# Optimization experiments

Measured on AMD Instinct MI355X. Metric: run time of the kernel, lower is better.

The kernel has to match this reference:

```python
import jax, jax.numpy as jnp
import numpy as np

P = 128; D = 128; A = 128
NS = D * A            # sinogram nodes
NP = P * P            # pixel nodes
N = NS + NP           # total graph nodes
EPS = 1e-5
_PNAMES = ["af_w1","af_b1","af_p1","af_bn_g","af_bn_b","af_w2","af_b2","af_p2","af_w3","af_b3","af_p3","af_w4","af_b4","af_p4","af_w5","af_b5","af_p5","gcn_w","gcn_b","sr_w1","sr_b1","sr_p1","sr_w2","sr_b2","sr_p2","sr_w3","sr_b3","sr_p3"]


def _conv(x, w, b, pad):
    y = jax.lax.conv_general_dilated(x, w, (1, 1), [(pad, pad), (pad, pad)],
                                     dimension_numbers=("NCHW", "OIHW", "NCHW"))
    return y + b[None, :, None, None]


def _prelu(x, a):
    return jnp.where(x >= 0, x, a * x)


def _bn(x, g, b):
    # BatchNorm2d in training mode: biased batch stats over (N,H,W)
    m = x.mean(axis=(0, 2, 3), keepdims=True)
    v = x.var(axis=(0, 2, 3), keepdims=True)
    return (x - m) * jax.lax.rsqrt(v + EPS) * g[None, :, None, None] + b[None, :, None, None]


def _forward(sino, edge_index, edge_weight, p):
    # AndrewCNN sinogram filter: 1 -> 64 -> 64 -> 64 -> 64 -> 8, 7x7 convs
    h = _prelu(_conv(sino, p["af_w1"], p["af_b1"], 3), p["af_p1"])
    h = _bn(h, p["af_bn_g"], p["af_bn_b"])
    h = _prelu(_conv(h, p["af_w2"], p["af_b2"], 3), p["af_p2"])
    h = _prelu(_conv(h, p["af_w3"], p["af_b3"], 3), p["af_p3"])
    h = _prelu(_conv(h, p["af_w4"], p["af_b4"], 3), p["af_p4"])
    h = _prelu(_conv(h, p["af_w5"], p["af_b5"], 3), p["af_p5"])   # [B,8,D,A]
    B, F = h.shape[0], h.shape[1]
    # build_nodes_features (source_to_target): sino nodes first, zero pixel nodes
    flat_sino = h.transpose(0, 2, 3, 1).reshape(B, NS, F)
    x = jnp.concatenate([flat_sino, jnp.zeros((B, NP, F), h.dtype)], axis=1)  # [B,N,8]
    # GCNConv(8,10): lin -> gcn_norm with self loops -> scatter-add at targets -> +bias
    xl = x @ p["gcn_w"]                                            # [B,N,10]
    row, col = edge_index[0], edge_index[1]
    loop = jnp.arange(N)
    row2 = jnp.concatenate([row, loop])
    col2 = jnp.concatenate([col, loop])
    w2 = jnp.concatenate([edge_weight, jnp.ones((N,), edge_weight.dtype)])
    deg = jnp.zeros((N,), xl.dtype).at[col2].add(w2)
    dis = jnp.where(deg > 0, jax.lax.rsqrt(jnp.maximum(deg, EPS * 0 + 1e-30)), 0.0)
    norm = dis[row2] * w2 * dis[col2]                              # [E+N]
    msgs = xl[:, row2, :] * norm[None, :, None]                    # [B,E+N,10]
    agg = jnp.zeros_like(xl).at[:, col2, :].add(msgs) + p["gcn_b"]
    # keep pixel nodes, reshape to image grid
    img = agg[:, NS:, :].transpose(0, 2, 1).reshape(B, -1, P, P)   # [B,10,P,P]
    # SRNET: 10 -> 64 (9x9) -> 32 (1x1) -> 1 (5x5)
    o = _prelu(_conv(img, p["sr_w1"], p["sr_b1"], 4), p["sr_p1"])
    o = _prelu(_conv(o,   p["sr_w2"], p["sr_b2"], 0), p["sr_p2"])
    o = _prelu(_conv(o,   p["sr_w3"], p["sr_b3"], 2), p["sr_p3"])
    return o


def setup_inputs() -> dict:
    f = jnp.float32
    ks = jax.random.split(jax.random.key(0), 16)
    B, E = 4, 2097152
    def rn(k, shape, s):
        return jax.random.normal(k, shape, f) * s
    inp = {
        "sino": jax.random.normal(ks[0], (B, 1, D, A), f),
        "edge_index": jax.random.randint(ks[1], (2, E), 0, N),
        "edge_weight": jax.random.uniform(ks[2], (E,), f),
    }
    kw = jax.random.split(ks[3], 9)
    inp["af_w1"] = rn(kw[0], (64, 1, 7, 7), 0.2)
    inp["af_w2"] = rn(kw[1], (64, 64, 7, 7), 0.03)
    inp["af_w3"] = rn(kw[2], (64, 64, 7, 7), 0.03)
    inp["af_w4"] = rn(kw[3], (64, 64, 7, 7), 0.03)
    inp["af_w5"] = rn(kw[4], (8, 64, 7, 7), 0.03)
    inp["gcn_w"] = rn(kw[5], (8, 10), 0.3)
    inp["sr_w1"] = rn(kw[6], (64, 10, 9, 9), 0.05)
    inp["sr_w2"] = rn(kw[7], (32, 64, 1, 1), 0.18)
    inp["sr_w3"] = rn(kw[8], (1, 32, 5, 5), 0.05)
    for nm, c in [("af_b1", 64), ("af_b2", 64), ("af_b3", 64), ("af_b4", 64), ("af_b5", 8), ("sr_b1", 64), ("sr_b2", 32), ("sr_b3", 1)]:
        inp[nm] = jnp.zeros((c,), f)
    inp["gcn_b"] = jnp.zeros((10,), f)
    inp["af_bn_g"] = jnp.ones((64,), f)
    inp["af_bn_b"] = jnp.zeros((64,), f)
    for nm in ["af_p1", "af_p2", "af_p3", "af_p4", "af_p5", "sr_p1", "sr_p2", "sr_p3"]:
        inp[nm] = jnp.array(0.25, f)
    return inp


def reference(sino, edge_index, edge_weight, af_w1, af_b1, af_p1, af_bn_g, af_bn_b, af_w2, af_b2, af_p2, af_w3, af_b3, af_p3, af_w4, af_b4, af_p4, af_w5, af_b5, af_p5, gcn_w, gcn_b, sr_w1, sr_b1, sr_p1, sr_w2, sr_b2, sr_p2, sr_w3, sr_b3, sr_p3):
    p = dict(zip(_PNAMES, (af_w1, af_b1, af_p1, af_bn_g, af_bn_b, af_w2, af_b2, af_p2, af_w3, af_b3, af_p3, af_w4, af_b4, af_p4, af_w5, af_b5, af_p5, gcn_w, gcn_b, sr_w1, sr_b1, sr_p1, sr_w2, sr_b2, sr_p2, sr_w3, sr_b3, sr_p3)))
    return _forward(sino, edge_index, edge_weight, p)
```

## Files before the change

kernel.cpp:

```cpp
#include <hip/hip_runtime.h>

static constexpr int NS = 16384;

typedef __attribute__((ext_vector_type(8))) short bf16x8;
typedef __attribute__((ext_vector_type(4))) float f32x4;

__device__ inline unsigned short bf16_rne(float x) {
  unsigned u = __float_as_uint(x);
  unsigned r = u + 0x7FFF + ((u >> 16) & 1);
  return (unsigned short)(r >> 16);
}

__global__ void k_wtrans(const float* __restrict__ w, float* __restrict__ wT,
                         int CO, int CI_IN, int CI_OUT, int KS) {
  int i = blockIdx.x * 256 + threadIdx.x;
  int tot = KS * KS * CI_OUT * CO;
  if (i >= tot) return;
  int co = i % CO;
  int r = i / CO;
  int ci = r % CI_OUT;
  int t = r / CI_OUT;
  int ky = t / KS, kx = t % KS;
  float v = 0.f;
  if (ci < CI_IN) v = w[((co * CI_IN + ci) * KS + ky) * KS + kx];
  wT[i] = v;
}

__global__ void k_wpack(const float* __restrict__ w, unsigned short* __restrict__ wpk) {
  int i = blockIdx.x * 256 + threadIdx.x;
  if (i >= 49 * 64 * 64) return;
  int co = i & 63, r = i >> 6;
  int ci = r & 63, tap = r >> 6;
  float v = w[(co * 64 + ci) * 49 + tap];
  unsigned short hi = bf16_rne(v);
  float hif = __uint_as_float((unsigned)hi << 16);
  unsigned short lo = bf16_rne(v - hif);
  int ks = ci >> 5, k32 = ci & 31;
  int lane = ((k32 >> 3) << 4) | (co & 15);
  int j = ci & 7, nt = co >> 4;
  size_t base = ((size_t)(((tap * 2 + ks) * 4 + nt) * 2) * 64 + lane) * 8 + j;
  wpk[base] = hi;
  wpk[base + 512] = lo;
}

__global__ void k_wpacks(const float* __restrict__ sw1,
                         unsigned short* __restrict__ wpk) {
  int i = blockIdx.x * 256 + threadIdx.x;
  if (i >= 360 * 512) return;
  int j = i & 7, l = (i >> 3) & 63, f = i >> 9;
  int sp = f & 1, nt = (f >> 1) & 3;
  int r3 = f >> 3, p = r3 % 5, ky = r3 / 5;
  int co = nt * 16 + (l & 15);
  int k = ((l >> 4) << 3) + j;
  int kx = 2 * p + (k >> 4);
  int ci = k & 15;
  float v = (ci < 10 && kx < 9) ? sw1[((co * 10 + ci) * 9 + ky) * 9 + kx] : 0.f;
  unsigned short hi = bf16_rne(v);
  unsigned short outv;
  if (sp == 0) {
    outv = hi;
  } else {
    float hif = __uint_as_float((unsigned)hi << 16);
    outv = bf16_rne(v - hif);
  }
  wpk[i] = outv;
}

__global__ __launch_bounds__(128) void k_conv1(
    const float* __restrict__ sino, const float* __restrict__ wT1,
    const float* __restrict__ b1, const float* __restrict__ p1,
    float* __restrict__ out) {
  int b = blockIdx.x >> 7, y = blockIdx.x & 127, x = threadIdx.x;
  float acc[64];
#pragma unroll
  for (int i = 0; i < 64; ++i) acc[i] = 0.f;
#pragma unroll
  for (int ky = 0; ky < 7; ++ky) {
    int yy = y + ky - 3;
#pragma unroll
    for (int kx = 0; kx < 7; ++kx) {
      int xx = x + kx - 3;
      float v = (yy >= 0 && yy < 128 && xx >= 0 && xx < 128)
                    ? sino[(b * 128 + yy) * 128 + xx]
                    : 0.f;
      const float* wr = wT1 + (ky * 7 + kx) * 64;
#pragma unroll
      for (int co = 0; co < 64; ++co) acc[co] += v * wr[co];
    }
  }
  float a = p1[0];
  float* op = out + ((size_t)(b * 134 + y + 3) * 134 + x + 3) * 64;
#pragma unroll
  for (int co = 0; co < 64; ++co) {
    float v = acc[co] + b1[co];
    op[co] = v >= 0.f ? v : a * v;
  }
}

__global__ __launch_bounds__(256) void k_bnstats(const float* __restrict__ x1p,
                                                 double* __restrict__ bnsum) {
  int c = threadIdx.x & 63, sl = threadIdx.x >> 6;
  double s = 0.0, q = 0.0;
  int base = blockIdx.x * 512 + sl * 128;
  for (int i = 0; i < 128; ++i) {
    int p = base + i;
    int b = p >> 14, y = (p >> 7) & 127, x = p & 127;
    double v = (double)x1p[((size_t)(b * 134 + y + 3) * 134 + x + 3) * 64 + c];
    s += v;
    q += v * v;
  }
  __shared__ double red[2][4][64];
  red[0][sl][c] = s;
  red[1][sl][c] = q;
  __syncthreads();
  if (sl == 0) {
    s = red[0][0][c] + red[0][1][c] + red[0][2][c] + red[0][3][c];
    q = red[1][0][c] + red[1][1][c] + red[1][2][c] + red[1][3][c];
    atomicAdd(&bnsum[c], s);
    atomicAdd(&bnsum[64 + c], q);
  }
}

__global__ void k_bnfinal(const double* __restrict__ bnsum, float* __restrict__ bnsc,
                          const float* __restrict__ g, const float* __restrict__ bb) {
  int c = threadIdx.x;
  if (c >= 64) return;
  double m = bnsum[c] * (1.0 / 65536.0);
  double v = bnsum[64 + c] * (1.0 / 65536.0) - m * m;
  double sc = (double)g[c] * rsqrt(v + 1e-5);
  bnsc[c] = (float)sc;
  bnsc[64 + c] = (float)((double)bb[c] - m * sc);
}

__global__ __launch_bounds__(256) void k_bnapply(float* __restrict__ x1p,
                                                 const float* __restrict__ bnsc) {
  int i = blockIdx.x * 256 + threadIdx.x;
  if (i >= 4 * 128 * 128 * 16) return;
  int g = i & 15, p = i >> 4;
  int b = p >> 14, y = (p >> 7) & 127, x = p & 127;
  float* ptr = x1p + ((size_t)(b * 134 + y + 3) * 134 + x + 3) * 64 + g * 4;
  float4 v = *(float4*)ptr;
  int c = g * 4;
  v.x = v.x * bnsc[c + 0] + bnsc[64 + c + 0];
  v.y = v.y * bnsc[c + 1] + bnsc[64 + c + 1];
  v.z = v.z * bnsc[c + 2] + bnsc[64 + c + 2];
  v.w = v.w * bnsc[c + 3] + bnsc[64 + c + 3];
  *(float4*)ptr = v;
}

__global__ __launch_bounds__(256) void k_convm(
    const float* __restrict__ in, const unsigned short* __restrict__ wpk,
    const float* __restrict__ bias, const float* __restrict__ alpha,
    float* __restrict__ out) {
  int b = blockIdx.x >> 7, y = blockIdx.x & 127;
  int tid = threadIdx.x, l = tid & 63;
  int wv = tid >> 6;
  int wbase = wv * 32;
  int lg = l >> 4, lm = l & 15;

  __shared__ unsigned short hbuf[2][134 * 40];
  __shared__ unsigned short lbuf[2][134 * 40];

  f32x4 acc[2][4];
#pragma unroll
  for (int mt = 0; mt < 2; ++mt)
#pragma unroll
    for (int nt = 0; nt < 4; ++nt) acc[mt][nt] = (f32x4){0.f, 0.f, 0.f, 0.f};

  for (int ch = 0; ch < 64; ch += 32) {
    auto stage = [&](int ky, int s) {
      const float* gin = in + ((size_t)(b * 134 + y + ky) * 134) * 64 + ch;
      for (int i = tid; i < 134 * 8; i += 256) {
        int px = i >> 3, q = i & 7;
        float4 v = *(const float4*)(gin + px * 64 + q * 4);
        unsigned short h0 = bf16_rne(v.x), h1 = bf16_rne(v.y);
        unsigned short h2 = bf16_rne(v.z), h3 = bf16_rne(v.w);
        unsigned short l0 = bf16_rne(v.x - __uint_as_float((unsigned)h0 << 16));
        unsigned short l1 = bf16_rne(v.y - __uint_as_float((unsigned)h1 << 16));
        unsigned short l2 = bf16_rne(v.z - __uint_as_float((unsigned)h2 << 16));
        unsigned short l3 = bf16_rne(v.w - __uint_as_float((unsigned)h3 << 16));
        *(ushort4*)&hbuf[s][px * 40 + q * 4] = make_ushort4(h0, h1, h2, h3);
        *(ushort4*)&lbuf[s][px * 40 + q * 4] = make_ushort4(l0, l1, l2, l3);
      }
    };
    stage(0, 0);
    __syncthreads();
    for (int ky = 0; ky < 7; ++ky) {
      if (ky < 6) stage(ky + 1, (ky + 1) & 1);
      int s = ky & 1;
#pragma unroll
      for (int kx = 0; kx < 7; ++kx) {
        int tap = ky * 7 + kx;
        const unsigned short* wt =
            wpk + (size_t)(tap * 2 + (ch >> 5)) * 8 * 512 + (size_t)l * 8;
        bf16x8 Bh[4], Bl[4];
#pragma unroll
        for (int nt = 0; nt < 4; ++nt) {
          Bh[nt] = *(const bf16x8*)(wt + (nt * 2 + 0) * 512);
          Bl[nt] = *(const bf16x8*)(wt + (nt * 2 + 1) * 512);
        }
#pragma unroll
        for (int mt = 0; mt < 2; ++mt) {
          int px = wbase + mt * 16 + lm + kx;
          bf16x8 Ah = *(const bf16x8*)&hbuf[s][px * 40 + lg * 8];
          bf16x8 Al = *(const bf16x8*)&lbuf[s][px * 40 + lg * 8];
#pragma unroll
          for (int nt = 0; nt < 4; ++nt) {
            acc[mt][nt] =
                __builtin_amdgcn_mfma_f32_16x16x32_bf16(Ah, Bh[nt], acc[mt][nt], 0, 0, 0);
            acc[mt][nt] =
                __builtin_amdgcn_mfma_f32_16x16x32_bf16(Ah, Bl[nt], acc[mt][nt], 0, 0, 0);
            acc[mt][nt] =
                __builtin_amdgcn_mfma_f32_16x16x32_bf16(Al, Bh[nt], acc[mt][nt], 0, 0, 0);
          }
        }
      }
      __syncthreads();
    }
  }
  float a = alpha[0];
#pragma unroll
  for (int mt = 0; mt < 2; ++mt)
#pragma unroll
    for (int nt = 0; nt < 4; ++nt)
#pragma unroll
      for (int r = 0; r < 4; ++r) {
        int px = wbase + mt * 16 + lg * 4 + r;
        int co = nt * 16 + lm;
        float v = acc[mt][nt][r] + bias[co];
        out[((size_t)(b * 134 + y + 3) * 134 + px + 3) * 64 + co] =
            v >= 0.f ? v : a * v;
      }
}

__global__ __launch_bounds__(256) void k_convs(
    const float* __restrict__ imgp, const unsigned short* __restrict__ wpk,
    const float* __restrict__ bias, const float* __restrict__ alpha,
    float* __restrict__ out) {
  int b = blockIdx.x >> 7, y = blockIdx.x & 127;
  int tid = threadIdx.x, l = tid & 63;
  int wv = tid >> 6, wbase = wv * 32;
  int lg = l >> 4, lm = l & 15;

  __shared__ unsigned short hbuf[2][137 * 20];
  __shared__ unsigned short lbuf[2][137 * 20];

  f32x4 acc[2][4];
#pragma unroll
  for (int mt = 0; mt < 2; ++mt)
#pragma unroll
    for (int nt = 0; nt < 4; ++nt) acc[mt][nt] = (f32x4){0.f, 0.f, 0.f, 0.f};

  auto stage = [&](int ky, int s) {
    const float* gin = imgp + ((size_t)(b * 136 + y + ky) * 136) * 16;
    for (int i = tid; i < 137 * 4; i += 256) {
      int px = i >> 2, q = i & 3;
      float4 v = (px < 136) ? *(const float4*)(gin + px * 16 + q * 4)
                            : make_float4(0.f, 0.f, 0.f, 0.f);
      unsigned short h0 = bf16_rne(v.x), h1 = bf16_rne(v.y);
      unsigned short h2 = bf16_rne(v.z), h3 = bf16_rne(v.w);
      unsigned short l0 = bf16_rne(v.x - __uint_as_float((unsigned)h0 << 16));
      unsigned short l1 = bf16_rne(v.y - __uint_as_float((unsigned)h1 << 16));
      unsigned short l2 = bf16_rne(v.z - __uint_as_float((unsigned)h2 << 16));
      unsigned short l3 = bf16_rne(v.w - __uint_as_float((unsigned)h3 << 16));
      *(ushort4*)&hbuf[s][px * 20 + q * 4] = make_ushort4(h0, h1, h2, h3);
      *(ushort4*)&lbuf[s][px * 20 + q * 4] = make_ushort4(l0, l1, l2, l3);
    }
  };
  stage(0, 0);
  __syncthreads();
  for (int ky = 0; ky < 9; ++ky) {
    if (ky < 8) stage(ky + 1, (ky + 1) & 1);
    int s = ky & 1;
#pragma unroll
    for (int p = 0; p < 5; ++p) {
      const unsigned short* wt =
          wpk + ((size_t)(ky * 5 + p) * 8) * 512 + (size_t)l * 8;
      bf16x8 Bh[4], Bl[4];
#pragma unroll
      for (int nt = 0; nt < 4; ++nt) {
        Bh[nt] = *(const bf16x8*)(wt + (nt * 2 + 0) * 512);
        Bl[nt] = *(const bf16x8*)(wt + (nt * 2 + 1) * 512);
      }
#pragma unroll
      for (int mt = 0; mt < 2; ++mt) {
        int px = wbase + mt * 16 + lm + 2 * p + (lg >> 1);
        bf16x8 Ah = *(const bf16x8*)&hbuf[s][px * 20 + (lg & 1) * 8];
        bf16x8 Al = *(const bf16x8*)&lbuf[s][px * 20 + (lg & 1) * 8];
#pragma unroll
        for (int nt = 0; nt < 4; ++nt) {
          acc[mt][nt] =
              __builtin_amdgcn_mfma_f32_16x16x32_bf16(Ah, Bh[nt], acc[mt][nt], 0, 0, 0);
          acc[mt][nt] =
              __builtin_amdgcn_mfma_f32_16x16x32_bf16(Ah, Bl[nt], acc[mt][nt], 0, 0, 0);
          acc[mt][nt] =
              __builtin_amdgcn_mfma_f32_16x16x32_bf16(Al, Bh[nt], acc[mt][nt], 0, 0, 0);
        }
      }
    }
    __syncthreads();
  }
  float a = alpha[0];
#pragma unroll
  for (int mt = 0; mt < 2; ++mt)
#pragma unroll
    for (int nt = 0; nt < 4; ++nt)
#pragma unroll
      for (int r = 0; r < 4; ++r) {
        int px = wbase + mt * 16 + lg * 4 + r;
        int co = nt * 16 + lm;
        float v = acc[mt][nt][r] + bias[co];
        out[((size_t)(b * 128 + y) * 128 + px) * 64 + co] = v >= 0.f ? v : a * v;
      }
}

template <int CIN, int COUT, int KS, int IN_H, int IN_W, int OUT_H, int OUT_W,
          int OUT_OFF, int STR, int CH, int NSPLIT>
__global__ __launch_bounds__(64 * NSPLIT) void k_conv3(
    const float* __restrict__ in, const float* __restrict__ wT,
    const float* __restrict__ bias, const float* __restrict__ alpha,
    float* __restrict__ out) {
  constexpr int C = COUT / NSPLIT;
  int b = blockIdx.x >> 6, y0 = (blockIdx.x & 63) * 2;
  int l = threadIdx.x & 63;
  int cob = __builtin_amdgcn_readfirstlane((int)(threadIdx.x >> 6) * C);
  __shared__ float sbuf[2][IN_W * STR];
  float acc[4][C];
#pragma unroll
  for (int r = 0; r < 4; ++r)
#pragma unroll
    for (int i = 0; i < C; ++i) acc[r][i] = 0.f;

  for (int ch = 0; ch < CIN; ch += CH) {
    auto stage = [&](int k) {
      const float* gin = in + ((size_t)(b * IN_H + y0 + k) * IN_W) * CIN + ch;
      float* dst = sbuf[k & 1];
      constexpr int N4 = IN_W * CH / 4;
      for (int i = threadIdx.x; i < N4; i += 64 * NSPLIT) {
        int xx = i / (CH / 4), c4 = (i - xx * (CH / 4)) * 4;
        float4 v = *(const float4*)(gin + (size_t)xx * CIN + c4);
        *(float4*)(dst + xx * STR + c4) = v;
      }
    };
    stage(0);
    stage(1);
    __syncthreads();
    for (int ky = 0; ky < KS; ++ky) {
      const float* sA = sbuf[ky & 1];
      const float* sB = sbuf[(ky + 1) & 1];
      for (int kx = 0; kx < KS; ++kx) {
        const float* wt = wT + ((size_t)(ky * KS + kx) * CIN + ch) * COUT + cob;
        const float* a0p = sA + (l + kx) * STR;
        const float* a1p = sA + (l + 64 + kx) * STR;
        const float* b0p = sB + (l + kx) * STR;
        const float* b1p = sB + (l + 64 + kx) * STR;
#pragma unroll
        for (int ci = 0; ci < CH; ci += 4) {
          float4 a0 = *(const float4*)(a0p + ci);
          float4 a1 = *(const float4*)(a1p + ci);
          float4 b0 = *(const float4*)(b0p + ci);
          float4 b1 = *(const float4*)(b1p + ci);
#pragma unroll
          for (int c = 0; c < 4; ++c) {
            const float* wr = wt + (size_t)(ci + c) * COUT;
            float va0 = ((const float*)&a0)[c], va1 = ((const float*)&a1)[c];
            float vb0 = ((const float*)&b0)[c], vb1 = ((const float*)&b1)[c];
#pragma unroll
            for (int co = 0; co < C; ++co) {
              float w = wr[co];
              acc[0][co] += va0 * w;
              acc[1][co] += va1 * w;
              acc[2][co] += vb0 * w;
              acc[3][co] += vb1 * w;
            }
          }
        }
      }
      __syncthreads();
      if (ky < KS - 1) {
        stage(ky + 2);
        __syncthreads();
      }
    }
  }
  float a = alpha[0];
#pragma unroll
  for (int r = 0; r < 2; ++r) {
    float* rowp =
        out + (((size_t)(b * OUT_H + y0 + r + OUT_OFF)) * OUT_W + OUT_OFF) * COUT + cob;
#pragma unroll
    for (int p = 0; p < 2; ++p) {
      float* op = rowp + (size_t)(l + p * 64) * COUT;
#pragma unroll
      for (int co = 0; co < C; ++co) {
        float v = acc[r * 2 + p][co] + bias[cob + co];
        op[co] = v >= 0.f ? v : a * v;
      }
    }
  }
}

template <int CIN, int COUT, int KS, int IN_H, int IN_W, int OUT_H, int OUT_W,
          int OUT_OFF, int STR, int NSPLIT>
__global__ __launch_bounds__(64 * NSPLIT) void k_conv2(
    const float* __restrict__ in, const float* __restrict__ wT,
    const float* __restrict__ bias, const float* __restrict__ alpha,
    float* __restrict__ out) {
  constexpr int C = COUT / NSPLIT;
  int b = blockIdx.x >> 7, y = blockIdx.x & 127;
  int l = threadIdx.x & 63;
  int cob = __builtin_amdgcn_readfirstlane((int)(threadIdx.x >> 6) * C);
  __shared__ float srow[IN_W * STR];
  float acc0[C], acc1[C];
#pragma unroll
  for (int i = 0; i < C; ++i) acc0[i] = acc1[i] = 0.f;

  for (int ky = 0; ky < KS; ++ky) {
    __syncthreads();
    const float* gin = in + (size_t)(b * IN_H + y + ky) * IN_W * CIN;
    constexpr int N4 = IN_W * CIN / 4;
    for (int i = threadIdx.x; i < N4; i += 64 * NSPLIT) {
      float4 v = *(const float4*)(gin + (size_t)i * 4);
      int xx = (i * 4) / CIN, cc = (i * 4) % CIN;
      *(float4*)(srow + xx * STR + cc) = v;
    }
    __syncthreads();
    for (int kx = 0; kx < KS; ++kx) {
      const float* wt = wT + ((size_t)(ky * KS + kx) * CIN) * COUT + cob;
      const float* s0 = srow + (l + kx) * STR;
      const float* s1 = srow + (l + 64 + kx) * STR;
      for (int ci = 0; ci < CIN; ci += 4) {
        float4 a0 = *(const float4*)(s0 + ci);
        float4 a1 = *(const float4*)(s1 + ci);
#pragma unroll
        for (int c = 0; c < 4; ++c) {
          float v0 = ((const float*)&a0)[c];
          float v1 = ((const float*)&a1)[c];
          const float* wr = wt + (size_t)(ci + c) * COUT;
#pragma unroll
          for (int co = 0; co < C; ++co) {
            float w = wr[co];
            acc0[co] += v0 * w;
            acc1[co] += v1 * w;
          }
        }
      }
    }
  }
  float a = alpha[0];
  float* rowp = out + ((size_t)(b * OUT_H + y + OUT_OFF) * OUT_W + OUT_OFF) * COUT + cob;
  float* op0 = rowp + (size_t)l * COUT;
  float* op1 = rowp + (size_t)(l + 64) * COUT;
#pragma unroll
  for (int co = 0; co < C; ++co) {
    float bi = bias[cob + co];
    float v0 = acc0[co] + bi;
    float v1 = acc1[co] + bi;
    op0[co] = v0 >= 0.f ? v0 : a * v0;
    op1[co] = v1 >= 0.f ? v1 : a * v1;
  }
}

__global__ __launch_bounds__(512, 4) void k_conv5gcn(
    const float* __restrict__ in, const float* __restrict__ wT5,
    const float* __restrict__ b5, const float* __restrict__ p5,
    const float* __restrict__ gw, float* __restrict__ xl) {
  int b = blockIdx.x >> 7, y = blockIdx.x & 127;
  int x = threadIdx.x & 127;
  int cig = __builtin_amdgcn_readfirstlane((int)(threadIdx.x >> 7));
  __shared__ float srow[134 * 68];
  __shared__ float red[4][128][8];
  float acc[8];
#pragma unroll
  for (int i = 0; i < 8; ++i) acc[i] = 0.f;

  for (int ky = 0; ky < 7; ++ky) {
    __syncthreads();
    const float* gin = in + (size_t)(b * 134 + y + ky) * 134 * 64;
    for (int i = threadIdx.x; i < 134 * 64; i += 512) {
      int xx = i >> 6, cc = i & 63;
      srow[xx * 68 + cc] = gin[i];
    }
    __syncthreads();
    for (int kx = 0; kx < 7; ++kx) {
      const float* wt = wT5 + (size_t)(ky * 7 + kx) * 64 * 8 + cig * 16 * 8;
      const float* sr = srow + (x + kx) * 68 + cig * 16;
#pragma unroll
      for (int ci = 0; ci < 16; ci += 4) {
        float4 iv = *(const float4*)(sr + ci);
#pragma unroll
        for (int c = 0; c < 4; ++c) {
          float vv = ((const float*)&iv)[c];
          const float* wr = wt + (ci + c) * 8;
#pragma unroll
          for (int co = 0; co < 8; ++co) acc[co] += vv * wr[co];
        }
      }
    }
  }
#pragma unroll
  for (int co = 0; co < 8; ++co) red[cig][x][co] = acc[co];
  __syncthreads();
  if (cig == 0) {
    float a = p5[0];
    float feat[8];
#pragma unroll
    for (int co = 0; co < 8; ++co) {
      float v = red[0][x][co] + red[1][x][co] + red[2][x][co] + red[3][x][co] + b5[co];
      feat[co] = v >= 0.f ? v : a * v;
    }
    float o[10];
#pragma unroll
    for (int f = 0; f < 10; ++f) o[f] = 0.f;
#pragma unroll
    for (int c = 0; c < 8; ++c) {
#pragma unroll
      for (int f = 0; f < 10; ++f) o[f] += feat[c] * gw[c * 10 + f];
    }
    float* op = xl + ((size_t)b * 16384 + y * 128 + x) * 10;
#pragma unroll
    for (int f = 0; f < 10; ++f) op[f] = o[f];
  }
}

__global__ void k_deg(const int* __restrict__ ei, const float* __restrict__ ew,
                      float* __restrict__ deg, int E) {
  int e = blockIdx.x * 256 + threadIdx.x;
  if (e >= E) return;
  atomicAdd(&deg[ei[E + e]], ew[e]);
}

__global__ void k_dis(const float* __restrict__ deg, float* __restrict__ dis) {
  int n = blockIdx.x * 256 + threadIdx.x;
  if (n >= 2 * NS) return;
  dis[n] = rsqrtf(deg[n] + 1.0f);
}

__global__ void k_hist(const int* __restrict__ ei, int* __restrict__ cnt, int E) {
  int e = blockIdx.x * 256 + threadIdx.x;
  if (e >= E) return;
  int row = ei[e], col = ei[E + e];
  if (row >= NS || col < NS) return;
  atomicAdd(&cnt[col - NS], 1);
}

__global__ __launch_bounds__(1024) void k_scan(const int* __restrict__ cnt,
                                               int* __restrict__ ptr) {
  __shared__ int ps[1024];
  int tid = threadIdx.x;
  int base = tid * 16;
  int v[16];
  int s = 0;
#pragma unroll
  for (int k = 0; k < 16; ++k) {
    v[k] = s;
    s += cnt[base + k];
  }
  ps[tid] = s;
  __syncthreads();
  for (int off = 1; off < 1024; off <<= 1) {
    int t = (tid >= off) ? ps[tid - off] : 0;
    __syncthreads();
    ps[tid] += t;
    __syncthreads();
  }
  int chunkoff = (tid == 0) ? 0 : ps[tid - 1];
#pragma unroll
  for (int k = 0; k < 16; ++k) ptr[base + k] = chunkoff + v[k];
  if (tid == 1023) ptr[16384] = ps[1023];
}

__global__ void k_bucket(const int* __restrict__ ei, const float* __restrict__ ew,
                         const float* __restrict__ dis, const int* __restrict__ ptr,
                         int* __restrict__ cur, int* __restrict__ erow,
                         float* __restrict__ enrm, int E) {
  int e = blockIdx.x * 256 + threadIdx.x;
  if (e >= E) return;
  int row = ei[e], col = ei[E + e];
  if (row >= NS || col < NS) return;
  int cp = col - NS;
  int pos = ptr[cp] + atomicAdd(&cur[cp], 1);
  erow[pos] = row;
  enrm[pos] = dis[row] * ew[e] * dis[col];
}

__global__ __launch_bounds__(256) void k_gather(
    const int* __restrict__ ptr, const int* __restrict__ erow,
    const float* __restrict__ enrm, const float* __restrict__ xl,
    const float* __restrict__ gb, float* __restrict__ imgp) {
  int cp = blockIdx.x * 4 + (threadIdx.x >> 6);
  int l = threadIdx.x & 63;
  int b = l >> 4, f = l & 15;
  bool act = f < 10;
  float acc = 0.f;
  int s = ptr[cp], e1 = ptr[cp + 1];
  for (int e = s; e < e1; ++e) {
    int row = erow[e];
    float nrm = enrm[e];
    if (act) acc += xl[((size_t)b * 16384 + row) * 10 + f] * nrm;
  }
  if (act) {
    int y = cp >> 7, x = cp & 127;
    imgp[((size_t)(b * 136 + y + 4) * 136 + x + 4) * 16 + f] = acc + gb[f];
  }
}

extern "C" void kernel_launch(void* const* d_in, const int* in_sizes, int n_in,
                              void* d_out, int out_size, void* d_ws, size_t ws_size,
                              hipStream_t stream) {
  const float* sino = (const float*)d_in[0];
  const int* ei = (const int*)d_in[1];
  const float* ew = (const float*)d_in[2];
  const float* w1 = (const float*)d_in[3];
  const float* w2 = (const float*)d_in[4];
  const float* w3 = (const float*)d_in[5];
  const float* w4 = (const float*)d_in[6];
  const float* w5 = (const float*)d_in[7];
  const float* gw = (const float*)d_in[8];
  const float* sw1 = (const float*)d_in[9];
  const float* sw2 = (const float*)d_in[10];
  const float* sw3 = (const float*)d_in[11];
  const float* b1 = (const float*)d_in[12];
  const float* b2 = (const float*)d_in[13];
  const float* b3 = (const float*)d_in[14];
  const float* b4 = (const float*)d_in[15];
  const float* b5 = (const float*)d_in[16];
  const float* sb1 = (const float*)d_in[17];
  const float* sb2 = (const float*)d_in[18];
  const float* sb3 = (const float*)d_in[19];
  const float* gb = (const float*)d_in[20];
  const float* bng = (const float*)d_in[21];
  const float* bnb = (const float*)d_in[22];
  const float* p1 = (const float*)d_in[23];
  const float* p2 = (const float*)d_in[24];
  const float* p3 = (const float*)d_in[25];
  const float* p4 = (const float*)d_in[26];
  const float* p5 = (const float*)d_in[27];
  const float* sp1 = (const float*)d_in[28];
  const float* sp2 = (const float*)d_in[29];
  const float* sp3 = (const float*)d_in[30];
  const int E = in_sizes[2];

  char* ws = (char*)d_ws;
  size_t off = 0;
  auto alloc = [&](size_t bytes) {
    char* p = ws + off;
    off += (bytes + 255) & ~(size_t)255;
    return p;
  };
  float* x1p = (float*)alloc((size_t)4 * 134 * 134 * 64 * 4);
  float* x2p = (float*)alloc((size_t)4 * 134 * 134 * 64 * 4);
  unsigned short* wpk2 = (unsigned short*)alloc(401408 * 2);
  unsigned short* wpk3 = (unsigned short*)alloc(401408 * 2);
  unsigned short* wpk4 = (unsigned short*)alloc(401408 * 2);
  unsigned short* wpks1 = (unsigned short*)alloc(184320 * 2);
  float* wt1 = (float*)alloc(3136 * 4);
  float* wt5 = (float*)alloc(25088 * 4);
  float* wts2 = (float*)alloc(2048 * 4);
  float* wts3 = (float*)alloc(800 * 4);
  double* bnsum = (double*)alloc(128 * 8);
  float* bnsc = (float*)alloc(128 * 4);
  float* xl = (float*)alloc((size_t)4 * 16384 * 10 * 4);
  float* deg = (float*)alloc(32768 * 4);
  float* dis = (float*)alloc(32768 * 4);
  int* cnt = (int*)alloc(16384 * 4);
  int* cur = (int*)alloc(16384 * 4);
  int* ptr = (int*)alloc(16385 * 4);
  int* erow = (int*)alloc((size_t)E * 4);
  float* enrm = (float*)alloc((size_t)E * 4);
  float* imgp = (float*)alloc((size_t)4 * 136 * 136 * 16 * 4);
  float* s1 = (float*)alloc((size_t)4 * 128 * 128 * 64 * 4);
  float* s2p = (float*)alloc((size_t)4 * 132 * 132 * 32 * 4);

  hipMemsetAsync(x1p, 0, (size_t)4 * 134 * 134 * 64 * 4, stream);
  hipMemsetAsync(x2p, 0, (size_t)4 * 134 * 134 * 64 * 4, stream);
  hipMemsetAsync(bnsum, 0, 128 * 8, stream);
  hipMemsetAsync(deg, 0, 32768 * 4, stream);
  hipMemsetAsync(cnt, 0, 16384 * 4, stream);
  hipMemsetAsync(cur, 0, 16384 * 4, stream);
  hipMemsetAsync(imgp, 0, (size_t)4 * 136 * 136 * 16 * 4, stream);
  hipMemsetAsync(s2p, 0, (size_t)4 * 132 * 132 * 32 * 4, stream);

  k_wpack<<<784, 256, 0, stream>>>(w2, wpk2);
  k_wpack<<<784, 256, 0, stream>>>(w3, wpk3);
  k_wpack<<<784, 256, 0, stream>>>(w4, wpk4);
  k_wpacks<<<720, 256, 0, stream>>>(sw1, wpks1);
  k_wtrans<<<13, 256, 0, stream>>>(w1, wt1, 64, 1, 1, 7);
  k_wtrans<<<98, 256, 0, stream>>>(w5, wt5, 8, 64, 64, 7);
  k_wtrans<<<8, 256, 0, stream>>>(sw2, wts2, 32, 64, 64, 1);
  k_wtrans<<<4, 256, 0, stream>>>(sw3, wts3, 1, 32, 32, 5);

  k_conv1<<<512, 128, 0, stream>>>(sino, wt1, b1, p1, x1p);
  k_bnstats<<<128, 256, 0, stream>>>(x1p, bnsum);
  k_bnfinal<<<1, 64, 0, stream>>>(bnsum, bnsc, bng, bnb);
  k_bnapply<<<4096, 256, 0, stream>>>(x1p, bnsc);

  k_convm<<<512, 256, 0, stream>>>(x1p, wpk2, b2, p2, x2p);
  k_convm<<<512, 256, 0, stream>>>(x2p, wpk3, b3, p3, x1p);
  k_convm<<<512, 256, 0, stream>>>(x1p, wpk4, b4, p4, x2p);
  k_conv5gcn<<<512, 512, 0, stream>>>(x2p, wt5, b5, p5, gw, xl);

  k_deg<<<(E + 255) / 256, 256, 0, stream>>>(ei, ew, deg, E);
  k_dis<<<128, 256, 0, stream>>>(deg, dis);
  k_hist<<<(E + 255) / 256, 256, 0, stream>>>(ei, cnt, E);
  k_scan<<<1, 1024, 0, stream>>>(cnt, ptr);
  k_bucket<<<(E + 255) / 256, 256, 0, stream>>>(ei, ew, dis, ptr, cur, erow, enrm, E);
  k_gather<<<4096, 256, 0, stream>>>(ptr, erow, enrm, xl, gb, imgp);

  k_convs<<<512, 256, 0, stream>>>(imgp, wpks1, sb1, sp1, s1);
  k_conv3<64, 32, 1, 128, 128, 132, 132, 2, 36, 32, 8>
      <<<256, 512, 0, stream>>>(s1, wts2, sb2, sp2, s2p);
  k_conv2<32, 1, 5, 132, 132, 128, 128, 0, 36, 1>
      <<<512, 64, 0, stream>>>(s2p, wts3, sb3, sp3, (float*)d_out);
}
```

Measured before the change: 761.7 us.

## Privatize degree accumulation in shared memory and precompute bucket ranks

After: 675.1 us. -11.4%, faster.

```diff
diff --git a/kernel.cpp b/kernel.cpp
--- a/kernel.cpp
+++ b/kernel.cpp
@@ -523,25 +523,38 @@
   }
 }
 
-__global__ void k_deg(const int* __restrict__ ei, const float* __restrict__ ew,
-                      float* __restrict__ deg, int E) {
-  int e = blockIdx.x * 256 + threadIdx.x;
-  if (e >= E) return;
-  atomicAdd(&deg[ei[E + e]], ew[e]);
-}
-
-__global__ void k_dis(const float* __restrict__ deg, float* __restrict__ dis) {
+template <int HALF>
+__global__ __launch_bounds__(1024) void k_degp(
+    const int* __restrict__ ei, const float* __restrict__ ew,
+    float* __restrict__ pdeg, int* __restrict__ cnt, int* __restrict__ rank, int E) {
+  __shared__ float degl[16384];
+  for (int i = threadIdx.x; i < 16384; i += 1024) degl[i] = 0.f;
+  __syncthreads();
+  int chunk = (E + gridDim.x - 1) / gridDim.x;
+  int base = blockIdx.x * chunk;
+  int end = min(E, base + chunk);
+  for (int e = base + (int)threadIdx.x; e < end; e += 1024) {
+    int col = ei[E + e];
+    float w = ew[e];
+    if ((col >> 14) == HALF) atomicAdd(&degl[col & 16383], w);
+    if (HALF == 1) {
+      int row = ei[e];
+      if (row < NS && col >= NS) rank[e] = atomicAdd(&cnt[col - NS], 1);
+    }
+  }
+  __syncthreads();
+  float* pd = pdeg + (size_t)blockIdx.x * 16384;
+  for (int i = threadIdx.x; i < 16384; i += 1024) pd[i] = degl[i];
+}
+
+__global__ void k_dis2(const float* __restrict__ pdegA, const float* __restrict__ pdegB,
+                       float* __restrict__ dis, int nb) {
   int n = blockIdx.x * 256 + threadIdx.x;
   if (n >= 2 * NS) return;
-  dis[n] = rsqrtf(deg[n] + 1.0f);
-}
-
-__global__ void k_hist(const int* __restrict__ ei, int* __restrict__ cnt, int E) {
-  int e = blockIdx.x * 256 + threadIdx.x;
-  if (e >= E) return;
-  int row = ei[e], col = ei[E + e];
-  if (row >= NS || col < NS) return;
-  atomicAdd(&cnt[col - NS], 1);
+  const float* p = (n < NS ? pdegA : pdegB) + (n & 16383);
+  float s = 1.0f;
+  for (int b = 0; b < nb; ++b) s += p[(size_t)b * 16384];
+  dis[n] = rsqrtf(s);
 }
 
 __global__ __launch_bounds__(1024) void k_scan(const int* __restrict__ cnt,
@@ -570,16 +583,16 @@
   if (tid == 1023) ptr[16384] = ps[1023];
 }
 
-__global__ void k_bucket(const int* __restrict__ ei, const float* __restrict__ ew,
-                         const float* __restrict__ dis, const int* __restrict__ ptr,
-                         int* __restrict__ cur, int* __restrict__ erow,
-                         float* __restrict__ enrm, int E) {
+__global__ void k_bucket2(const int* __restrict__ ei, const float* __restrict__ ew,
+                          const float* __restrict__ dis, const int* __restrict__ ptr,
+                          const int* __restrict__ rank, int* __restrict__ erow,
+                          float* __restrict__ enrm, int E) {
   int e = blockIdx.x * 256 + threadIdx.x;
   if (e >= E) return;
   int row = ei[e], col = ei[E + e];
   if (row >= NS || col < NS) return;
   int cp = col - NS;
-  int pos = ptr[cp] + atomicAdd(&cur[cp], 1);
+  int pos = ptr[cp] + rank[e];
   erow[pos] = row;
   enrm[pos] = dis[row] * ew[e] * dis[col];
 }
@@ -661,11 +674,12 @@
   double* bnsum = (double*)alloc(128 * 8);
   float* bnsc = (float*)alloc(128 * 4);
   float* xl = (float*)alloc((size_t)4 * 16384 * 10 * 4);
-  float* deg = (float*)alloc(32768 * 4);
+  float* pdegA = (float*)alloc((size_t)128 * 16384 * 4);
+  float* pdegB = (float*)alloc((size_t)128 * 16384 * 4);
   float* dis = (float*)alloc(32768 * 4);
   int* cnt = (int*)alloc(16384 * 4);
-  int* cur = (int*)alloc(16384 * 4);
   int* ptr = (int*)alloc(16385 * 4);
+  int* rank = (int*)alloc((size_t)E * 4);
   int* erow = (int*)alloc((size_t)E * 4);
   float* enrm = (float*)alloc((size_t)E * 4);
   float* imgp = (float*)alloc((size_t)4 * 136 * 136 * 16 * 4);
@@ -675,9 +689,7 @@
   hipMemsetAsync(x1p, 0, (size_t)4 * 134 * 134 * 64 * 4, stream);
   hipMemsetAsync(x2p, 0, (size_t)4 * 134 * 134 * 64 * 4, stream);
   hipMemsetAsync(bnsum, 0, 128 * 8, stream);
-  hipMemsetAsync(deg, 0, 32768 * 4, stream);
   hipMemsetAsync(cnt, 0, 16384 * 4, stream);
-  hipMemsetAsync(cur, 0, 16384 * 4, stream);
   hipMemsetAsync(imgp, 0, (size_t)4 * 136 * 136 * 16 * 4, stream);
   hipMemsetAsync(s2p, 0, (size_t)4 * 132 * 132 * 32 * 4, stream);
 
@@ -700,11 +712,11 @@
   k_convm<<<512, 256, 0, stream>>>(x1p, wpk4, b4, p4, x2p);
   k_conv5gcn<<<512, 512, 0, stream>>>(x2p, wt5, b5, p5, gw, xl);
 
-  k_deg<<<(E + 255) / 256, 256, 0, stream>>>(ei, ew, deg, E);
-  k_dis<<<128, 256, 0, stream>>>(deg, dis);
-  k_hist<<<(E + 255) / 256, 256, 0, stream>>>(ei, cnt, E);
+  k_degp<0><<<128, 1024, 0, stream>>>(ei, ew, pdegA, cnt, rank, E);
+  k_degp<1><<<128, 1024, 0, stream>>>(ei, ew, pdegB, cnt, rank, E);
+  k_dis2<<<128, 256, 0, stream>>>(pdegA, pdegB, dis, 128);
   k_scan<<<1, 1024, 0, stream>>>(cnt, ptr);
-  k_bucket<<<(E + 255) / 256, 256, 0, stream>>>(ei, ew, dis, ptr, cur, erow, enrm, E);
+  k_bucket2<<<(E + 255) / 256, 256, 0, stream>>>(ei, ew, dis, ptr, rank, erow, enrm, E);
   k_gather<<<4096, 256, 0, stream>>>(ptr, erow, enrm, xl, gb, imgp);
 
   k_convs<<<512, 256, 0, stream>>>(imgp, wpks1, sb1, sp1, s1);
```
